# Performance work log

Hardware: AMD Instinct MI355X
Metric: run time of the kernel (lower is better)

## Reference

```python
import jax, jax.numpy as jnp
import numpy as np

B, S, D = 2, 2048, 1024
H = 16
HD = D // H
SCALE = float(np.sqrt(HD))


def setup_inputs() -> dict:
    key = jax.random.key(0)
    ks = jax.random.split(key, 10)
    def lin(k):
        # xavier_uniform for [out, in] = [D, D]
        bound = float(np.sqrt(6.0 / (D + D)))
        return jax.random.uniform(k, (D, D), jnp.float32, -bound, bound)
    return {
        "hidden_states": jax.random.normal(ks[0], (B, S, D), jnp.float32),
        "attention_mask": jnp.ones((B, S), jnp.float32),
        "Wq": lin(ks[1]), "bq": jnp.zeros((D,), jnp.float32),
        "Wk": lin(ks[2]), "bk": jnp.zeros((D,), jnp.float32),
        "Wv": lin(ks[3]), "bv": jnp.zeros((D,), jnp.float32),
        "Wo": lin(ks[4]), "bo": jnp.zeros((D,), jnp.float32),
    }


def _heads(x):
    # [B,S,D] -> [B,H,S,HD]
    return x.reshape(B, S, H, HD).transpose(0, 2, 1, 3)


def secure_softmax(scores):
    c = jnp.clip(scores, -3.0, 3.0)
    sig = 0.5 + 0.25 * c - 0.01 * c ** 3
    sig = jnp.clip(sig, 0.01, 0.99)
    return sig / (jnp.sum(sig, axis=-1, keepdims=True) + 1e-8)


def reference(hidden_states, attention_mask, Wq, bq, Wk, bk, Wv, bv, Wo, bo):
    q = _heads(hidden_states @ Wq.T + bq)
    k = _heads(hidden_states @ Wk.T + bk)
    v = _heads(hidden_states @ Wv.T + bv)
    # [B,H,S,S]
    scores = jnp.einsum("bhqd,bhkd->bhqk", q, k) / SCALE
    scores = scores + (1.0 - attention_mask[:, None, None, :]) * -10000.0
    probs = secure_softmax(scores)
    ctx = jnp.einsum("bhqk,bhkd->bhqd", probs, v)
    ctx = ctx.transpose(0, 2, 1, 3).reshape(B, S, D)
    return ctx @ Wo.T + bo
```

## Files before the change

### kernel.cpp

```cpp
#include <hip/hip_runtime.h>
#include <stdint.h>

#define B_ 2
#define S_ 2048
#define D_ 1024
#define H_ 16
#define HD_ 64
#define M_ (B_*S_)

typedef __bf16 bf16;
typedef __attribute__((ext_vector_type(8))) __bf16 bf16x8;
typedef __attribute__((ext_vector_type(4))) float f32x4;

__device__ __forceinline__ void gload16(const bf16* g, bf16* l) {
    __builtin_amdgcn_global_load_lds(
        (const __attribute__((address_space(1))) void*)g,
        (__attribute__((address_space(3))) void*)l, 16, 0, 0);
}

__global__ void k_cvt(const float* __restrict__ src, bf16* __restrict__ dst, int n) {
    int idx = (blockIdx.x * blockDim.x + threadIdx.x) * 8;
    if (idx < n) {
        float4 a = *(const float4*)(src + idx);
        float4 b = *(const float4*)(src + idx + 4);
        bf16 o[8] = {(bf16)a.x,(bf16)a.y,(bf16)a.z,(bf16)a.w,
                     (bf16)b.x,(bf16)b.y,(bf16)b.z,(bf16)b.w};
        *(int4*)(dst + idx) = *(const int4*)o;
    }
}

__global__ void k_cvt4(const float* __restrict__ s0, const float* __restrict__ s1,
                       const float* __restrict__ s2, const float* __restrict__ s3,
                       bf16* __restrict__ d0, bf16* __restrict__ d1,
                       bf16* __restrict__ d2, bf16* __restrict__ d3) {
    const float* s = (blockIdx.y==0)?s0:(blockIdx.y==1)?s1:(blockIdx.y==2)?s2:s3;
    bf16* d = (blockIdx.y==0)?d0:(blockIdx.y==1)?d1:(blockIdx.y==2)?d2:d3;
    int idx = (blockIdx.x * blockDim.x + threadIdx.x) * 8;
    float4 a = *(const float4*)(s + idx);
    float4 b = *(const float4*)(s + idx + 4);
    bf16 o[8] = {(bf16)a.x,(bf16)a.y,(bf16)a.z,(bf16)a.w,
                 (bf16)b.x,(bf16)b.y,(bf16)b.z,(bf16)b.w};
    *(int4*)(d + idx) = *(const int4*)o;
}

__global__ __launch_bounds__(256) void k_gemm_qkv(
    const bf16* __restrict__ X,
    const bf16* __restrict__ Wq, const bf16* __restrict__ Wk, const bf16* __restrict__ Wv,
    const float* __restrict__ bq, const float* __restrict__ bk, const float* __restrict__ bv,
    bf16* __restrict__ Qo, bf16* __restrict__ Ko, bf16* __restrict__ Vo)
{
    const int z = blockIdx.z;
    const bf16* W = (z==0) ? Wq : (z==1) ? Wk : Wv;
    const float* bias = (z==0) ? bq : (z==1) ? bk : bv;
    const int n0 = blockIdx.x * 128;
    const int m0 = blockIdx.y * 128;
    const int t = threadIdx.x;
    const int w = t >> 6, lane = t & 63, quad = lane >> 4, l15 = lane & 15;
    const int lr = lane >> 3;
    const int lc = (lane & 7) ^ lr;
    const int sx = l15 & 7;
    const int mw = (w >> 1) * 64, nw = (w & 1) * 64;

    __shared__ __align__(16) bf16 As[128*64];
    __shared__ __align__(16) bf16 Bs[128*64];

    f32x4 acc[4][4];
    #pragma unroll
    for (int i = 0; i < 4; i++)
        #pragma unroll
        for (int j = 0; j < 4; j++)
            acc[i][j] = (f32x4){0.f,0.f,0.f,0.f};

    const bf16* gA = X + (size_t)(m0 + w*8 + lr)*D_ + lc*8;
    const bf16* gB = W + (size_t)(n0 + w*8 + lr)*D_ + lc*8;

    for (int k0 = 0; k0 < D_; k0 += 64) {
        #pragma unroll
        for (int c = 0; c < 4; c++) {
            gload16(gA + (size_t)c*32*D_ + k0, &As[c*2048 + w*512]);
            gload16(gB + (size_t)c*32*D_ + k0, &Bs[c*2048 + w*512]);
        }
        __syncthreads();
        #pragma unroll
        for (int ks = 0; ks < 2; ks++) {
            bf16x8 af[4], bfr[4];
            #pragma unroll
            for (int i = 0; i < 4; i++)
                af[i] = *(const bf16x8*)&As[(mw + i*16 + l15)*64 + (((ks*4+quad)^sx)*8)];
            #pragma unroll
            for (int j = 0; j < 4; j++)
                bfr[j] = *(const bf16x8*)&Bs[(nw + j*16 + l15)*64 + (((ks*4+quad)^sx)*8)];
            #pragma unroll
            for (int i = 0; i < 4; i++)
                #pragma unroll
                for (int j = 0; j < 4; j++)
                    acc[i][j] = __builtin_amdgcn_mfma_f32_16x16x32_bf16(af[i], bfr[j], acc[i][j], 0, 0, 0);
        }
        __syncthreads();
    }

    const float scale = (z == 0) ? 0.125f : 1.0f;
    #pragma unroll
    for (int j = 0; j < 4; j++) {
        int n = n0 + nw + j*16 + l15;
        float bn = bias[n];
        int h = n >> 6, hd = n & 63;
        #pragma unroll
        for (int i = 0; i < 4; i++) {
            int mbase = m0 + mw + i*16 + quad*4;
            int b = mbase >> 11;
            int sbase = mbase & 2047;
            if (z == 2) {
                union { bf16 h4[4]; uint2 u; } pk;
                #pragma unroll
                for (int r = 0; r < 4; r++) pk.h4[r] = (bf16)(acc[i][j][r] + bn);
                *(uint2*)&Vo[((size_t)((b*H_ + h)*HD_ + hd))*S_ + sbase] = pk.u;
            } else {
                bf16* Out = (z == 0) ? Qo : Ko;
                #pragma unroll
                for (int r = 0; r < 4; r++) {
                    int s = sbase + r;
                    Out[((size_t)((b*H_ + h)*S_ + s))*HD_ + hd] = (bf16)((acc[i][j][r] + bn) * scale);
                }
            }
        }
    }
}

__global__ __launch_bounds__(256) void k_gemm_out(
    const bf16* __restrict__ X, const bf16* __restrict__ W,
    const float* __restrict__ bias, float* __restrict__ Out)
{
    const int n0 = blockIdx.x * 128;
    const int m0 = blockIdx.y * 64;
    const int t = threadIdx.x;
    const int w = t >> 6, lane = t & 63, quad = lane >> 4, l15 = lane & 15;
    const int lr = lane >> 3;
    const int lc = (lane & 7) ^ lr;
    const int sx = l15 & 7;
    const int nw = w * 32;

    __shared__ __align__(16) bf16 As[64*64];
    __shared__ __align__(16) bf16 Bs[128*64];

    f32x4 acc[4][2];
    #pragma unroll
    for (int i = 0; i < 4; i++)
        #pragma unroll
        for (int j = 0; j < 2; j++)
            acc[i][j] = (f32x4){0.f,0.f,0.f,0.f};

    const bf16* gA = X + (size_t)(m0 + w*8 + lr)*D_ + lc*8;
    const bf16* gB = W + (size_t)(n0 + w*8 + lr)*D_ + lc*8;

    for (int k0 = 0; k0 < D_; k0 += 64) {
        #pragma unroll
        for (int c = 0; c < 2; c++)
            gload16(gA + (size_t)c*32*D_ + k0, &As[c*2048 + w*512]);
        #pragma unroll
        for (int c = 0; c < 4; c++)
            gload16(gB + (size_t)c*32*D_ + k0, &Bs[c*2048 + w*512]);
        __syncthreads();
        #pragma unroll
        for (int ks = 0; ks < 2; ks++) {
            bf16x8 af[4], bfr[2];
            #pragma unroll
            for (int i = 0; i < 4; i++)
                af[i] = *(const bf16x8*)&As[(i*16 + l15)*64 + (((ks*4+quad)^sx)*8)];
            #pragma unroll
            for (int j = 0; j < 2; j++)
                bfr[j] = *(const bf16x8*)&Bs[(nw + j*16 + l15)*64 + (((ks*4+quad)^sx)*8)];
            #pragma unroll
            for (int i = 0; i < 4; i++)
                #pragma unroll
                for (int j = 0; j < 2; j++)
                    acc[i][j] = __builtin_amdgcn_mfma_f32_16x16x32_bf16(af[i], bfr[j], acc[i][j], 0, 0, 0);
        }
        __syncthreads();
    }

    #pragma unroll
    for (int j = 0; j < 2; j++) {
        int n = n0 + nw + j*16 + l15;
        float bn = bias[n];
        #pragma unroll
        for (int i = 0; i < 4; i++) {
            int mbase = m0 + i*16 + quad*4;
            #pragma unroll
            for (int r = 0; r < 4; r++)
                Out[(size_t)(mbase + r)*D_ + n] = acc[i][j][r] + bn;
        }
    }
}

__global__ __launch_bounds__(256) void k_attn(
    const bf16* __restrict__ Q, const bf16* __restrict__ K, const bf16* __restrict__ Vt,
    const float* __restrict__ mask, bf16* __restrict__ Ctx)
{
    const int bh = blockIdx.y;
    const int b = bh >> 4, h = bh & 15;
    const int q0 = blockIdx.x * 64;
    const int t = threadIdx.x;
    const int w = t >> 6, lane = t & 63, quad = lane >> 4, l15 = lane & 15;
    const int lr = lane >> 3;
    const int lc = (lane & 7) ^ lr;
    const int sx = l15 & 7;

    __shared__ __align__(16) bf16 Qs[64*64];
    __shared__ __align__(16) bf16 Ks[64*64];
    __shared__ __align__(16) bf16 Vs[64*64];
    __shared__ __align__(16) bf16 Ps[64*64];
    __shared__ float mts[64];
    __shared__ float lsum[64];

    const bf16* Qg = Q + ((size_t)bh*S_ + q0 + w*8 + lr)*HD_ + lc*8;
    #pragma unroll
    for (int c = 0; c < 2; c++)
        gload16(Qg + (size_t)c*32*HD_, &Qs[c*2048 + w*512]);
    __syncthreads();

    bf16x8 bq[2];
    #pragma unroll
    for (int ks = 0; ks < 2; ks++)
        bq[ks] = *(const bf16x8*)&Qs[(w*16 + l15)*64 + (((ks*4+quad)^sx)*8)];

    f32x4 cacc[4];
    #pragma unroll
    for (int j = 0; j < 4; j++) cacc[j] = (f32x4){0.f,0.f,0.f,0.f};
    float lac = 0.f;

    const bf16* Kst = K + ((size_t)bh*S_ + w*8 + lr)*HD_ + lc*8;
    const bf16* Vst = Vt + ((size_t)bh*HD_ + w*8 + lr)*S_ + lc*8;

    for (int it = 0; it < S_/64; it++) {
        const int k0 = it*64;
        #pragma unroll
        for (int c = 0; c < 2; c++)
            gload16(Kst + (size_t)(k0 + c*32)*HD_, &Ks[c*2048 + w*512]);
        #pragma unroll
        for (int c = 0; c < 2; c++)
            gload16(Vst + (size_t)c*32*S_ + k0, &Vs[c*2048 + w*512]);
        if (t < 64) mts[t] = (1.0f - mask[(size_t)b*S_ + k0 + t]) * -10000.0f;
        __syncthreads();

        f32x4 st[4];
        #pragma unroll
        for (int mt = 0; mt < 4; mt++) st[mt] = (f32x4){0.f,0.f,0.f,0.f};
        #pragma unroll
        for (int ks = 0; ks < 2; ks++) {
            bf16x8 af[4];
            #pragma unroll
            for (int mt = 0; mt < 4; mt++)
                af[mt] = *(const bf16x8*)&Ks[(mt*16 + l15)*64 + (((ks*4+quad)^sx)*8)];
            #pragma unroll
            for (int mt = 0; mt < 4; mt++)
                st[mt] = __builtin_amdgcn_mfma_f32_16x16x32_bf16(af[mt], bq[ks], st[mt], 0, 0, 0);
        }

        #pragma unroll
        for (int mt = 0; mt < 4; mt++) {
            float4 m4 = *(const float4*)&mts[mt*16 + quad*4];
            float mv[4] = {m4.x, m4.y, m4.z, m4.w};
            union { bf16 h4[4]; uint2 u; } pk;
            #pragma unroll
            for (int r = 0; r < 4; r++) {
                float s = st[mt][r] + mv[r];
                float c = __builtin_amdgcn_fmed3f(s, -3.0f, 3.0f);
                float u = fmaf(c*c, -0.01f, 0.25f);
                float sg = fmaf(c, u, 0.5f);
                sg = __builtin_amdgcn_fmed3f(sg, 0.01f, 0.99f);
                lac += sg;
                pk.h4[r] = (bf16)sg;
            }
            int c8 = (mt*2 + (quad>>1)) ^ sx;
            *(uint2*)&Ps[(w*16 + l15)*64 + c8*8 + (quad&1)*4] = pk.u;
        }
        __syncthreads();

        #pragma unroll
        for (int ks = 0; ks < 2; ks++) {
            bf16x8 pf, vf[4];
            pf = *(const bf16x8*)&Ps[(w*16 + l15)*64 + (((ks*4+quad)^sx)*8)];
            #pragma unroll
            for (int nt = 0; nt < 4; nt++)
                vf[nt] = *(const bf16x8*)&Vs[(nt*16 + l15)*64 + (((ks*4+quad)^sx)*8)];
            #pragma unroll
            for (int nt = 0; nt < 4; nt++)
                cacc[nt] = __builtin_amdgcn_mfma_f32_16x16x32_bf16(pf, vf[nt], cacc[nt], 0, 0, 0);
        }
        __syncthreads();
    }

    {
        float v = lac;
        v += __shfl_xor(v, 16);
        v += __shfl_xor(v, 32);
        if (quad == 0) lsum[w*16 + l15] = v;
    }
    __syncthreads();

    #pragma unroll
    for (int r = 0; r < 4; r++) {
        int q = w*16 + quad*4 + r;
        float rinv = 1.0f / (lsum[q] + 1e-8f);
        size_t row = (size_t)(b*S_ + q0 + q);
        #pragma unroll
        for (int nt = 0; nt < 4; nt++)
            Ctx[row*D_ + h*HD_ + nt*16 + l15] = (bf16)(cacc[nt][r] * rinv);
    }
}

extern "C" void kernel_launch(void* const* d_in, const int* in_sizes, int n_in,
                              void* d_out, int out_size, void* d_ws, size_t ws_size,
                              hipStream_t stream) {
    const float* hs   = (const float*)d_in[0];
    const float* mask = (const float*)d_in[1];
    const float* Wq   = (const float*)d_in[2];
    const float* bq   = (const float*)d_in[3];
    const float* Wk   = (const float*)d_in[4];
    const float* bk   = (const float*)d_in[5];
    const float* Wv   = (const float*)d_in[6];
    const float* bv   = (const float*)d_in[7];
    const float* Wo   = (const float*)d_in[8];
    const float* bo   = (const float*)d_in[9];
    float* out = (float*)d_out;

    char* ws = (char*)d_ws;
    const size_t MB = 1024*1024;
    bf16* hb   = (bf16*)(ws);
    bf16* wqb  = (bf16*)(ws + 8*MB);
    bf16* wkb  = (bf16*)(ws + 10*MB);
    bf16* wvb  = (bf16*)(ws + 12*MB);
    bf16* wob  = (bf16*)(ws + 14*MB);
    bf16* qb   = (bf16*)(ws + 16*MB);
    bf16* kb   = (bf16*)(ws + 24*MB);
    bf16* vtb  = (bf16*)(ws + 32*MB);
    bf16* ctxb = (bf16*)(ws + 40*MB);

    k_cvt<<<M_*D_/2048, 256, 0, stream>>>(hs, hb, M_*D_);
    k_cvt4<<<dim3(D_*D_/2048, 4), 256, 0, stream>>>(Wq, Wk, Wv, Wo, wqb, wkb, wvb, wob);

    k_gemm_qkv<<<dim3(D_/128, M_/128, 3), 256, 0, stream>>>(
        hb, wqb, wkb, wvb, bq, bk, bv, qb, kb, vtb);

    k_attn<<<dim3(S_/64, B_*H_), 256, 0, stream>>>(qb, kb, vtb, mask, ctxb);

    k_gemm_out<<<dim3(D_/128, M_/64), 256, 0, stream>>>(ctxb, wob, bo, out);
}
```

Before: 215.7 us.

## Enlarge attention query tile, double-buffer K/V, stage QKV epilogue through LDS

The attention kernel now handles 128 queries per block, keeps Q fragments in registers, and splits the work across waves by key rows instead of query rows. K/V tiles are double-buffered so the next tile's loads overlap the current compute, and the mask is read directly from global memory. The QKV GEMM epilogue stages results through shared memory so the transposed Q/K/V stores become coalesced 16-byte writes, and the two convert kernels are merged into one launch. The cost is more register pressure from the Q fragments and eight accumulators, a cross-wave row-sum reduction, and extra LDS traffic in the epilogue.

```diff
diff --git a/kernel.cpp b/kernel.cpp
--- a/kernel.cpp
+++ b/kernel.cpp
@@ -18,24 +18,21 @@
         (__attribute__((address_space(3))) void*)l, 16, 0, 0);
 }
 
-__global__ void k_cvt(const float* __restrict__ src, bf16* __restrict__ dst, int n) {
-    int idx = (blockIdx.x * blockDim.x + threadIdx.x) * 8;
-    if (idx < n) {
-        float4 a = *(const float4*)(src + idx);
-        float4 b = *(const float4*)(src + idx + 4);
-        bf16 o[8] = {(bf16)a.x,(bf16)a.y,(bf16)a.z,(bf16)a.w,
-                     (bf16)b.x,(bf16)b.y,(bf16)b.z,(bf16)b.w};
-        *(int4*)(dst + idx) = *(const int4*)o;
-    }
-}
-
-__global__ void k_cvt4(const float* __restrict__ s0, const float* __restrict__ s1,
-                       const float* __restrict__ s2, const float* __restrict__ s3,
-                       bf16* __restrict__ d0, bf16* __restrict__ d1,
-                       bf16* __restrict__ d2, bf16* __restrict__ d3) {
-    const float* s = (blockIdx.y==0)?s0:(blockIdx.y==1)?s1:(blockIdx.y==2)?s2:s3;
-    bf16* d = (blockIdx.y==0)?d0:(blockIdx.y==1)?d1:(blockIdx.y==2)?d2:d3;
-    int idx = (blockIdx.x * blockDim.x + threadIdx.x) * 8;
+__global__ void k_cvt_all(const float* __restrict__ hs,
+                          const float* __restrict__ Wq, const float* __restrict__ Wk,
+                          const float* __restrict__ Wv, const float* __restrict__ Wo,
+                          bf16* __restrict__ hb,
+                          bf16* __restrict__ wqb, bf16* __restrict__ wkb,
+                          bf16* __restrict__ wvb, bf16* __restrict__ wob) {
+    int blk = blockIdx.x;
+    const float* s; bf16* d; int base;
+    if (blk < 2048) { s = hs; d = hb; base = blk; }
+    else {
+        int r = blk - 2048; int which = r >> 9; base = r & 511;
+        s = (which==0)?Wq:(which==1)?Wk:(which==2)?Wv:Wo;
+        d = (which==0)?wqb:(which==1)?wkb:(which==2)?wvb:wob;
+    }
+    int idx = base*2048 + threadIdx.x*8;
     float4 a = *(const float4*)(s + idx);
     float4 b = *(const float4*)(s + idx + 4);
     bf16 o[8] = {(bf16)a.x,(bf16)a.y,(bf16)a.z,(bf16)a.w,
@@ -61,8 +58,10 @@
     const int sx = l15 & 7;
     const int mw = (w >> 1) * 64, nw = (w & 1) * 64;
 
-    __shared__ __align__(16) bf16 As[128*64];
-    __shared__ __align__(16) bf16 Bs[128*64];
+    __shared__ __align__(16) char smraw[128*136*2];
+    bf16* As  = (bf16*)smraw;
+    bf16* Bs  = (bf16*)(smraw + 16384);
+    bf16* epi = (bf16*)smraw;
 
     f32x4 acc[4][4];
     #pragma unroll
@@ -100,29 +99,57 @@
     }
 
     const float scale = (z == 0) ? 0.125f : 1.0f;
-    #pragma unroll
-    for (int j = 0; j < 4; j++) {
-        int n = n0 + nw + j*16 + l15;
-        float bn = bias[n];
-        int h = n >> 6, hd = n & 63;
-        #pragma unroll
-        for (int i = 0; i < 4; i++) {
-            int mbase = m0 + mw + i*16 + quad*4;
-            int b = mbase >> 11;
-            int sbase = mbase & 2047;
-            if (z == 2) {
+    if (z == 2) {
+        #pragma unroll
+        for (int j = 0; j < 4; j++) {
+            int n = nw + j*16 + l15;
+            float bn = bias[n0 + n];
+            #pragma unroll
+            for (int i = 0; i < 4; i++) {
+                int mloc = mw + i*16 + quad*4;
                 union { bf16 h4[4]; uint2 u; } pk;
                 #pragma unroll
                 for (int r = 0; r < 4; r++) pk.h4[r] = (bf16)(acc[i][j][r] + bn);
-                *(uint2*)&Vo[((size_t)((b*H_ + h)*HD_ + hd))*S_ + sbase] = pk.u;
-            } else {
-                bf16* Out = (z == 0) ? Qo : Ko;
-                #pragma unroll
-                for (int r = 0; r < 4; r++) {
-                    int s = sbase + r;
-                    Out[((size_t)((b*H_ + h)*S_ + s))*HD_ + hd] = (bf16)((acc[i][j][r] + bn) * scale);
-                }
+                *(uint2*)&epi[n*136 + mloc] = pk.u;
             }
+        }
+    } else {
+        #pragma unroll
+        for (int j = 0; j < 4; j++) {
+            int n = nw + j*16 + l15;
+            float bn = bias[n0 + n];
+            #pragma unroll
+            for (int i = 0; i < 4; i++) {
+                int mloc = mw + i*16 + quad*4;
+                #pragma unroll
+                for (int r = 0; r < 4; r++)
+                    epi[(mloc + r)*136 + n] = (bf16)((acc[i][j][r] + bn) * scale);
+            }
+        }
+    }
+    __syncthreads();
+    if (z == 2) {
+        #pragma unroll
+        for (int kk = 0; kk < 8; kk++) {
+            int c = t + 256*kk;
+            int row = c >> 4;
+            int mcol = (c & 15) * 8;
+            int4 val = *(const int4*)&epi[row*136 + mcol];
+            int n = n0 + row; int hh = n >> 6, hd = n & 63;
+            int m = m0 + mcol; int bb = m >> 11, s = m & 2047;
+            *(int4*)&Vo[((size_t)((bb*H_ + hh)*HD_ + hd))*S_ + s] = val;
+        }
+    } else {
+        bf16* Out = (z == 0) ? Qo : Ko;
+        #pragma unroll
+        for (int kk = 0; kk < 8; kk++) {
+            int c = t + 256*kk;
+            int row = c >> 4;
+            int ncol = (c & 15) * 8;
+            int4 val = *(const int4*)&epi[row*136 + ncol];
+            int m = m0 + row; int bb = m >> 11, s = m & 2047;
+            int n = n0 + ncol; int hh = n >> 6, hd = n & 63;
+            *(int4*)&Out[((size_t)((bb*H_ + hh)*S_ + s))*HD_ + hd] = val;
         }
     }
 }
@@ -193,120 +220,138 @@
     }
 }
 
-__global__ __launch_bounds__(256) void k_attn(
+__global__ __launch_bounds__(256, 2) void k_attn(
     const bf16* __restrict__ Q, const bf16* __restrict__ K, const bf16* __restrict__ Vt,
     const float* __restrict__ mask, bf16* __restrict__ Ctx)
 {
     const int bh = blockIdx.y;
     const int b = bh >> 4, h = bh & 15;
-    const int q0 = blockIdx.x * 64;
+    const int q0 = blockIdx.x * 128;
     const int t = threadIdx.x;
     const int w = t >> 6, lane = t & 63, quad = lane >> 4, l15 = lane & 15;
     const int lr = lane >> 3;
     const int lc = (lane & 7) ^ lr;
     const int sx = l15 & 7;
 
-    __shared__ __align__(16) bf16 Qs[64*64];
-    __shared__ __align__(16) bf16 Ks[64*64];
-    __shared__ __align__(16) bf16 Vs[64*64];
-    __shared__ __align__(16) bf16 Ps[64*64];
-    __shared__ float mts[64];
-    __shared__ float lsum[64];
-
-    const bf16* Qg = Q + ((size_t)bh*S_ + q0 + w*8 + lr)*HD_ + lc*8;
-    #pragma unroll
-    for (int c = 0; c < 2; c++)
-        gload16(Qg + (size_t)c*32*HD_, &Qs[c*2048 + w*512]);
-    __syncthreads();
-
-    bf16x8 bq[2];
-    #pragma unroll
-    for (int ks = 0; ks < 2; ks++)
-        bq[ks] = *(const bf16x8*)&Qs[(w*16 + l15)*64 + (((ks*4+quad)^sx)*8)];
-
-    f32x4 cacc[4];
-    #pragma unroll
-    for (int j = 0; j < 4; j++) cacc[j] = (f32x4){0.f,0.f,0.f,0.f};
-    float lac = 0.f;
+    __shared__ __align__(16) bf16 Ks[2][64*64];
+    __shared__ __align__(16) bf16 Vs[2][64*64];
+    __shared__ __align__(16) bf16 Ps[128*64];
+    __shared__ float lsumP[4][128];
+
+    bf16x8 qf[8][2];
+    const bf16* Qbase = Q + ((size_t)bh*S_ + q0)*HD_;
+    #pragma unroll
+    for (int qs = 0; qs < 8; qs++)
+        #pragma unroll
+        for (int ks = 0; ks < 2; ks++)
+            qf[qs][ks] = *(const bf16x8*)&Qbase[(size_t)(qs*16 + l15)*HD_ + ks*32 + quad*8];
+
+    f32x4 cacc[2][4];
+    #pragma unroll
+    for (int i = 0; i < 2; i++)
+        #pragma unroll
+        for (int j = 0; j < 4; j++)
+            cacc[i][j] = (f32x4){0.f,0.f,0.f,0.f};
+    float lac[8];
+    #pragma unroll
+    for (int qs = 0; qs < 8; qs++) lac[qs] = 0.f;
 
     const bf16* Kst = K + ((size_t)bh*S_ + w*8 + lr)*HD_ + lc*8;
     const bf16* Vst = Vt + ((size_t)bh*HD_ + w*8 + lr)*S_ + lc*8;
 
+    #pragma unroll
+    for (int c = 0; c < 2; c++)
+        gload16(Kst + (size_t)c*32*HD_, &Ks[0][c*2048 + w*512]);
+    #pragma unroll
+    for (int c = 0; c < 2; c++)
+        gload16(Vst + (size_t)c*32*S_, &Vs[0][c*2048 + w*512]);
+    __syncthreads();
+
     for (int it = 0; it < S_/64; it++) {
+        const int cur = it & 1;
         const int k0 = it*64;
-        #pragma unroll
-        for (int c = 0; c < 2; c++)
-            gload16(Kst + (size_t)(k0 + c*32)*HD_, &Ks[c*2048 + w*512]);
-        #pragma unroll
-        for (int c = 0; c < 2; c++)
-            gload16(Vst + (size_t)c*32*S_ + k0, &Vs[c*2048 + w*512]);
-        if (t < 64) mts[t] = (1.0f - mask[(size_t)b*S_ + k0 + t]) * -10000.0f;
-        __syncthreads();
-
-        f32x4 st[4];
-        #pragma unroll
-        for (int mt = 0; mt < 4; mt++) st[mt] = (f32x4){0.f,0.f,0.f,0.f};
+
+        f32x4 st[8];
+        #pragma unroll
+        for (int qs = 0; qs < 8; qs++) st[qs] = (f32x4){0.f,0.f,0.f,0.f};
         #pragma unroll
         for (int ks = 0; ks < 2; ks++) {
-            bf16x8 af[4];
-            #pragma unroll
-            for (int mt = 0; mt < 4; mt++)
-                af[mt] = *(const bf16x8*)&Ks[(mt*16 + l15)*64 + (((ks*4+quad)^sx)*8)];
-            #pragma unroll
-            for (int mt = 0; mt < 4; mt++)
-                st[mt] = __builtin_amdgcn_mfma_f32_16x16x32_bf16(af[mt], bq[ks], st[mt], 0, 0, 0);
-        }
-
-        #pragma unroll
-        for (int mt = 0; mt < 4; mt++) {
-            float4 m4 = *(const float4*)&mts[mt*16 + quad*4];
-            float mv[4] = {m4.x, m4.y, m4.z, m4.w};
+            bf16x8 af = *(const bf16x8*)&Ks[cur][(w*16 + l15)*64 + (((ks*4+quad)^sx)*8)];
+            #pragma unroll
+            for (int qs = 0; qs < 8; qs++)
+                st[qs] = __builtin_amdgcn_mfma_f32_16x16x32_bf16(af, qf[qs][ks], st[qs], 0, 0, 0);
+        }
+
+        float4 m4 = *(const float4*)&mask[(size_t)b*S_ + k0 + w*16 + quad*4];
+        float mv[4] = {(1.0f-m4.x)*-10000.0f, (1.0f-m4.y)*-10000.0f,
+                       (1.0f-m4.z)*-10000.0f, (1.0f-m4.w)*-10000.0f};
+        const int c8 = (w*2 + (quad>>1)) ^ sx;
+        #pragma unroll
+        for (int qs = 0; qs < 8; qs++) {
             union { bf16 h4[4]; uint2 u; } pk;
             #pragma unroll
             for (int r = 0; r < 4; r++) {
-                float s = st[mt][r] + mv[r];
+                float s = st[qs][r] + mv[r];
                 float c = __builtin_amdgcn_fmed3f(s, -3.0f, 3.0f);
                 float u = fmaf(c*c, -0.01f, 0.25f);
                 float sg = fmaf(c, u, 0.5f);
                 sg = __builtin_amdgcn_fmed3f(sg, 0.01f, 0.99f);
-                lac += sg;
+                lac[qs] += sg;
                 pk.h4[r] = (bf16)sg;
             }
-            int c8 = (mt*2 + (quad>>1)) ^ sx;
-            *(uint2*)&Ps[(w*16 + l15)*64 + c8*8 + (quad&1)*4] = pk.u;
-        }
-        __syncthreads();
+            *(uint2*)&Ps[(qs*16 + l15)*64 + c8*8 + (quad&1)*4] = pk.u;
+        }
+        __syncthreads();
+
+        if (it < S_/64 - 1) {
+            const int nxt = cur ^ 1, k1 = k0 + 64;
+            #pragma unroll
+            for (int c = 0; c < 2; c++)
+                gload16(Kst + (size_t)(k1 + c*32)*HD_, &Ks[nxt][c*2048 + w*512]);
+            #pragma unroll
+            for (int c = 0; c < 2; c++)
+                gload16(Vst + (size_t)c*32*S_ + k1, &Vs[nxt][c*2048 + w*512]);
+        }
 
         #pragma unroll
         for (int ks = 0; ks < 2; ks++) {
-            bf16x8 pf, vf[4];
-            pf = *(const bf16x8*)&Ps[(w*16 + l15)*64 + (((ks*4+quad)^sx)*8)];
+            bf16x8 pf[2], vf[4];
+            #pragma unroll
+            for (int m2 = 0; m2 < 2; m2++)
+                pf[m2] = *(const bf16x8*)&Ps[(w*32 + m2*16 + l15)*64 + (((ks*4+quad)^sx)*8)];
             #pragma unroll
             for (int nt = 0; nt < 4; nt++)
-                vf[nt] = *(const bf16x8*)&Vs[(nt*16 + l15)*64 + (((ks*4+quad)^sx)*8)];
-            #pragma unroll
-            for (int nt = 0; nt < 4; nt++)
-                cacc[nt] = __builtin_amdgcn_mfma_f32_16x16x32_bf16(pf, vf[nt], cacc[nt], 0, 0, 0);
-        }
-        __syncthreads();
-    }
-
-    {
-        float v = lac;
+                vf[nt] = *(const bf16x8*)&Vs[cur][(nt*16 + l15)*64 + (((ks*4+quad)^sx)*8)];
+            #pragma unroll
+            for (int m2 = 0; m2 < 2; m2++)
+                #pragma unroll
+                for (int nt = 0; nt < 4; nt++)
+                    cacc[m2][nt] = __builtin_amdgcn_mfma_f32_16x16x32_bf16(pf[m2], vf[nt], cacc[m2][nt], 0, 0, 0);
+        }
+        __syncthreads();
+    }
+
+    #pragma unroll
+    for (int qs = 0; qs < 8; qs++) {
+        float v = lac[qs];
         v += __shfl_xor(v, 16);
         v += __shfl_xor(v, 32);
-        if (quad == 0) lsum[w*16 + l15] = v;
+        if (quad == 0) lsumP[w][qs*16 + l15] = v;
     }
     __syncthreads();
 
     #pragma unroll
-    for (int r = 0; r < 4; r++) {
-        int q = w*16 + quad*4 + r;
-        float rinv = 1.0f / (lsum[q] + 1e-8f);
-        size_t row = (size_t)(b*S_ + q0 + q);
-        #pragma unroll
-        for (int nt = 0; nt < 4; nt++)
-            Ctx[row*D_ + h*HD_ + nt*16 + l15] = (bf16)(cacc[nt][r] * rinv);
+    for (int m2 = 0; m2 < 2; m2++) {
+        #pragma unroll
+        for (int r = 0; r < 4; r++) {
+            int q = w*32 + m2*16 + quad*4 + r;
+            float s = lsumP[0][q] + lsumP[1][q] + lsumP[2][q] + lsumP[3][q];
+            float rinv = 1.0f / (s + 1e-8f);
+            size_t row = (size_t)(b*S_ + q0 + q);
+            #pragma unroll
+            for (int nt = 0; nt < 4; nt++)
+                Ctx[row*D_ + h*HD_ + nt*16 + l15] = (bf16)(cacc[m2][nt][r] * rinv);
+        }
     }
 }
 
@@ -337,13 +382,12 @@
     bf16* vtb  = (bf16*)(ws + 32*MB);
     bf16* ctxb = (bf16*)(ws + 40*MB);
 
-    k_cvt<<<M_*D_/2048, 256, 0, stream>>>(hs, hb, M_*D_);
-    k_cvt4<<<dim3(D_*D_/2048, 4), 256, 0, stream>>>(Wq, Wk, Wv, Wo, wqb, wkb, wvb, wob);
+    k_cvt_all<<<2048 + 4*512, 256, 0, stream>>>(hs, Wq, Wk, Wv, Wo, hb, wqb, wkb, wvb, wob);
 
     k_gemm_qkv<<<dim3(D_/128, M_/128, 3), 256, 0, stream>>>(
         hb, wqb, wkb, wvb, bq, bk, bv, qb, kb, vtb);
 
-    k_attn<<<dim3(S_/64, B_*H_), 256, 0, stream>>>(qb, kb, vtb, mask, ctxb);
+    k_attn<<<dim3(S_/128, B_*H_), 256, 0, stream>>>(qb, kb, vtb, mask, ctxb);
 
     k_gemm_out<<<dim3(D_/128, M_/64), 256, 0, stream>>>(ctxb, wob, bo, out);
 }
```

New measurement: 209.4 us. -2.9%, faster.
